# Optimization experiments

Hardware: AMD Instinct MI355X
Metric: run time of the kernel (lower is better)

Reference implementation:

```python
import jax, jax.numpy as jnp
import numpy as np
from jax import lax

C = 320
GN_GROUPS = 32
EPS = 1e-5


def setup_inputs() -> dict:
    key = jax.random.key(0)
    ks = jax.random.split(key, 5)
    x = jax.random.normal(ks[0], (16, C, 96, 96), dtype=jnp.float32)
    # depthwise 3x3 kernel [C,1,3,3] (OIHW with feature_group_count=C)
    dw_w = jax.random.normal(ks[1], (C, 1, 3, 3), dtype=jnp.float32) * 0.1
    dw_b = jax.random.normal(ks[2], (C,), dtype=jnp.float32) * 0.01
    gn_w = jnp.ones((C,), dtype=jnp.float32)
    gn_b = jnp.zeros((C,), dtype=jnp.float32)
    proj_w = jax.random.normal(ks[3], (C,), dtype=jnp.float32) * 0.001
    proj_b = jnp.full((1,), -4.0, dtype=jnp.float32)
    return {"x": x, "dw_w": dw_w, "dw_b": dw_b, "gn_w": gn_w,
            "gn_b": gn_b, "proj_w": proj_w, "proj_b": proj_b}


def _group_norm(h, gamma, beta):
    # h: [B,C,H,W]; GN over (C//G, H, W) within each of G groups; biased var (torch)
    B, Cc, H, W = h.shape
    hg = h.reshape(B, GN_GROUPS, Cc // GN_GROUPS, H, W)
    mean = jnp.mean(hg, axis=(2, 3, 4), keepdims=True)
    var = jnp.mean(jnp.square(hg - mean), axis=(2, 3, 4), keepdims=True)
    hn = ((hg - mean) * lax.rsqrt(var + EPS)).reshape(B, Cc, H, W)
    return hn * gamma[None, :, None, None] + beta[None, :, None, None]


def reference(x, dw_w, dw_b, gn_w, gn_b, proj_w, proj_b):
    # depthwise 3x3 conv, padding=1
    h = lax.conv_general_dilated(
        x, dw_w, window_strides=(1, 1), padding=((1, 1), (1, 1)),
        dimension_numbers=("NCHW", "OIHW", "NCHW"), feature_group_count=C)
    h = h + dw_b[None, :, None, None]
    h = _group_norm(h, gn_w, gn_b)
    # 1x1 conv C -> 1 == per-pixel channel dot product
    g = jnp.einsum("bchw,c->bhw", h, proj_w) + proj_b[0]
    return jax.nn.sigmoid(g)[:, None, :, :]  # [B,1,H,W]
```

## Files before the change

kernel.cpp:

```cpp
#include <hip/hip_runtime.h>
#include <math.h>

#define HH 96
#define WW 96
#define NPIX (HH*WW)
#define CC 320
#define GG 32
#define CPG 10
#define TPB 512

typedef _Float16 half4v __attribute__((ext_vector_type(4)));

__global__ __launch_bounds__(TPB, 4)
void k_main(const float* __restrict__ x, const float* __restrict__ dw_w,
            const float* __restrict__ dw_b, const float* __restrict__ gn_w,
            const float* __restrict__ proj_w,
            _Float16* __restrict__ P, float* __restrict__ partials) {
  const int gr = blockIdx.x & 31;
  const int b  = blockIdx.x >> 5;

  __shared__ float wsm[CPG * 9], ssm[CPG], bsm[CPG];
  const int tid = threadIdx.x;
  if (tid < CPG * 9) wsm[tid] = dw_w[gr * CPG * 9 + tid];
  if (tid < CPG) {
    int c = gr * CPG + tid;
    ssm[tid] = proj_w[c] * gn_w[c];
    bsm[tid] = dw_b[c];
  }
  __syncthreads();

  const int lane = tid & 63;
  const int xcl  = tid & 31;
  const int r    = tid >> 5;
  const bool active = xcl < 24;
  const float mact  = active ? 1.f : 0.f;
  const int xc = min(xcl, 23);
  const float mlft = (xcl > 0)  ? 1.f : 0.f;
  const float mrgt = (xcl < 23) ? 1.f : 0.f;
  const int lm1 = (xcl >= 1) ? lane - 1 : lane;
  const int lp1 = (xcl < 31) ? lane + 1 : lane;

  const float mtop = (r > 0)  ? 1.f : 0.f;
  const float mbot = (r < 15) ? 1.f : 0.f;

  int offs[8];
  #pragma unroll
  for (int k = 0; k < 8; ++k) {
    int yy = min(max(6 * r - 1 + k, 0), HH - 1);
    offs[k] = yy * WW + xc * 4;
  }
  const float* xg = x + ((size_t)(b * CC + gr * CPG)) * NPIX;

  float p[24];
  #pragma unroll
  for (int i = 0; i < 24; ++i) p[i] = 0.f;
  float s1 = 0.f, s2 = 0.f;

  #pragma unroll 1
  for (int ch = 0; ch < CPG; ++ch) {
    const float* img = xg + ch * NPIX;

    float4 R[8];
    #pragma unroll
    for (int k = 0; k < 8; ++k) R[k] = *(const float4*)(img + offs[k]);
    R[0].x *= mtop; R[0].y *= mtop; R[0].z *= mtop; R[0].w *= mtop;
    R[7].x *= mbot; R[7].y *= mbot; R[7].z *= mbot; R[7].w *= mbot;

    float L[8], T[8];
    #pragma unroll
    for (int k = 0; k < 8; ++k) {
      L[k] = __shfl(R[k].w, lm1) * mlft;
      T[k] = __shfl(R[k].x, lp1) * mrgt;
    }

    const float* wp = &wsm[ch * 9];
    const float w0 = wp[0], w1 = wp[1], w2 = wp[2];
    const float w3 = wp[3], w4 = wp[4], w5 = wp[5];
    const float w6 = wp[6], w7 = wp[7], w8 = wp[8];
    const float sc = ssm[ch], bias = bsm[ch];

    #pragma unroll
    for (int j = 0; j < 6; ++j) {
      const float4 A = R[j], B = R[j + 1], C = R[j + 2];
      const float la = L[j], lb = L[j + 1], lc = L[j + 2];
      const float ta = T[j], tb = T[j + 1], tc = T[j + 2];

      float u0 = w0*la  + w1*A.x + w2*A.y + w3*lb  + w4*B.x + w5*B.y + w6*lc  + w7*C.x + w8*C.y;
      float u1 = w0*A.x + w1*A.y + w2*A.z + w3*B.x + w4*B.y + w5*B.z + w6*C.x + w7*C.y + w8*C.z;
      float u2 = w0*A.y + w1*A.z + w2*A.w + w3*B.y + w4*B.z + w5*B.w + w6*C.y + w7*C.z + w8*C.w;
      float u3 = w0*A.z + w1*A.w + w2*ta  + w3*B.z + w4*B.w + w5*tb  + w6*C.z + w7*C.w + w8*tc;

      p[j*4+0] = fmaf(sc, u0, p[j*4+0]);
      p[j*4+1] = fmaf(sc, u1, p[j*4+1]);
      p[j*4+2] = fmaf(sc, u2, p[j*4+2]);
      p[j*4+3] = fmaf(sc, u3, p[j*4+3]);

      float h0 = u0 + bias, h1 = u1 + bias, h2 = u2 + bias, h3 = u3 + bias;
      s1 += mact * ((h0 + h1) + (h2 + h3));
      s2 += mact * (fmaf(h0, h0, h1 * h1) + fmaf(h2, h2, h3 * h3));
    }
  }

  if (active) {
    _Float16* Pp = P + ((size_t)(b * GG + gr)) * NPIX;
    #pragma unroll
    for (int j = 0; j < 6; ++j) {
      half4v h;
      h.x = (_Float16)p[j*4+0]; h.y = (_Float16)p[j*4+1];
      h.z = (_Float16)p[j*4+2]; h.w = (_Float16)p[j*4+3];
      *(half4v*)&Pp[(size_t)(6 * r + j) * WW + xcl * 4] = h;
    }
  }

  #pragma unroll
  for (int off = 32; off; off >>= 1) {
    s1 += __shfl_down(s1, off);
    s2 += __shfl_down(s2, off);
  }
  __shared__ float r1[8], r2[8];
  if ((tid & 63) == 0) { r1[tid >> 6] = s1; r2[tid >> 6] = s2; }
  __syncthreads();
  if (tid == 0) {
    float a = 0.f, q = 0.f;
    #pragma unroll
    for (int i = 0; i < 8; ++i) { a += r1[i]; q += r2[i]; }
    partials[blockIdx.x * 2]     = a;
    partials[blockIdx.x * 2 + 1] = q;
  }
}

__global__ __launch_bounds__(128)
void k_out(const _Float16* __restrict__ P, const float* __restrict__ partials,
           const float* __restrict__ dw_b, const float* __restrict__ gn_w,
           const float* __restrict__ gn_b, const float* __restrict__ proj_w,
           const float* __restrict__ proj_b, float* __restrict__ out) {
  const int b   = blockIdx.x / 18;
  const int blk = blockIdx.x % 18;
  __shared__ float rs[GG];
  __shared__ float Ds;

  if (threadIdx.x < GG) {
    const int gr = threadIdx.x;
    float s1 = partials[(b * GG + gr) * 2];
    float s2 = partials[(b * GG + gr) * 2 + 1];
    const float invN = 1.f / (float)(CPG * NPIX);
    float mean = s1 * invN;
    float var  = s2 * invN - mean * mean;
    float rinv = rsqrtf(var + 1e-5f);
    rs[gr] = rinv;
    float K = 0.f, E = 0.f;
    #pragma unroll
    for (int i = 0; i < CPG; ++i) {
      int c = gr * CPG + i;
      float pg = proj_w[c] * gn_w[c];
      K = fmaf(pg, dw_b[c] - mean, K);
      E = fmaf(proj_w[c], gn_b[c], E);
    }
    float contrib = fmaf(rinv, K, E);
    #pragma unroll
    for (int m = 16; m; m >>= 1) contrib += __shfl_xor(contrib, m, 32);
    if (gr == 0) Ds = contrib + proj_b[0];
  }
  __syncthreads();

  const int p = (blk * 128 + threadIdx.x) * 4;
  const _Float16* Pb = P + (size_t)b * GG * NPIX + p;
  float g0 = 0.f, g1 = 0.f, g2 = 0.f, g3 = 0.f;
  #pragma unroll
  for (int gr = 0; gr < GG; ++gr) {
    half4v v = *(const half4v*)(Pb + (size_t)gr * NPIX);
    float rr = rs[gr];
    g0 = fmaf(rr, (float)v.x, g0);
    g1 = fmaf(rr, (float)v.y, g1);
    g2 = fmaf(rr, (float)v.z, g2);
    g3 = fmaf(rr, (float)v.w, g3);
  }
  const float d = Ds;
  float4 o;
  o.x = 1.f / (1.f + expf(-(g0 + d)));
  o.y = 1.f / (1.f + expf(-(g1 + d)));
  o.z = 1.f / (1.f + expf(-(g2 + d)));
  o.w = 1.f / (1.f + expf(-(g3 + d)));
  *(float4*)&out[(size_t)b * NPIX + p] = o;
}

extern "C" void kernel_launch(void* const* d_in, const int* in_sizes, int n_in,
                              void* d_out, int out_size, void* d_ws, size_t ws_size,
                              hipStream_t stream) {
  const float* x      = (const float*)d_in[0];
  const float* dw_w   = (const float*)d_in[1];
  const float* dw_b   = (const float*)d_in[2];
  const float* gn_w   = (const float*)d_in[3];
  const float* gn_b   = (const float*)d_in[4];
  const float* proj_w = (const float*)d_in[5];
  const float* proj_b = (const float*)d_in[6];
  float* out = (float*)d_out;

  const size_t P_BYTES = (size_t)16 * GG * NPIX * 2;
  _Float16* P     = (_Float16*)d_ws;
  float* partials = (float*)((char*)d_ws + P_BYTES);

  hipLaunchKernelGGL(k_main, dim3(16 * GG), dim3(TPB), 0, stream,
                     x, dw_w, dw_b, gn_w, proj_w, P, partials);
  hipLaunchKernelGGL(k_out, dim3(16 * 18), dim3(128), 0, stream,
                     P, partials, dw_b, gn_w, gn_b, proj_w, proj_b, out);
}
```

Measured before the change: 52.21 us.

## Fuse main and output kernels with a global atomic grid barrier

Merges the two kernels into one and separates the stages with a device-wide atomic counter barrier, which a memset resets before each launch. After the barrier every block computes the group-norm scale factors for its batch and writes 288 output pixels. This removes the second launch and its tail gap. It depends on all 512 blocks being co-resident to avoid deadlock, and the output phase now reads fp16 values as scalars instead of half4 vectors.

After: 146.6 us. 181% more time.

```diff
diff --git a/kernel.cpp b/kernel.cpp
--- a/kernel.cpp
+++ b/kernel.cpp
@@ -8,18 +8,25 @@
 #define GG 32
 #define CPG 10
 #define TPB 512
+#define NBLK (16*GG)
 
 typedef _Float16 half4v __attribute__((ext_vector_type(4)));
 
 __global__ __launch_bounds__(TPB, 4)
-void k_main(const float* __restrict__ x, const float* __restrict__ dw_w,
-            const float* __restrict__ dw_b, const float* __restrict__ gn_w,
-            const float* __restrict__ proj_w,
-            _Float16* __restrict__ P, float* __restrict__ partials) {
+void k_fused(const float* __restrict__ x, const float* __restrict__ dw_w,
+             const float* __restrict__ dw_b, const float* __restrict__ gn_w,
+             const float* __restrict__ gn_b, const float* __restrict__ proj_w,
+             const float* __restrict__ proj_b,
+             _Float16* __restrict__ P, float* __restrict__ partials,
+             unsigned int* __restrict__ bar, float* __restrict__ out) {
   const int gr = blockIdx.x & 31;
   const int b  = blockIdx.x >> 5;
 
   __shared__ float wsm[CPG * 9], ssm[CPG], bsm[CPG];
+  __shared__ float r1[8], r2[8];
+  __shared__ float rs[GG];
+  __shared__ float Ds;
+
   const int tid = threadIdx.x;
   if (tid < CPG * 9) wsm[tid] = dw_w[gr * CPG * 9 + tid];
   if (tid < CPG) {
@@ -39,7 +46,6 @@
   const float mrgt = (xcl < 23) ? 1.f : 0.f;
   const int lm1 = (xcl >= 1) ? lane - 1 : lane;
   const int lp1 = (xcl < 31) ? lane + 1 : lane;
-
   const float mtop = (r > 0)  ? 1.f : 0.f;
   const float mbot = (r < 15) ? 1.f : 0.f;
 
@@ -59,7 +65,6 @@
   #pragma unroll 1
   for (int ch = 0; ch < CPG; ++ch) {
     const float* img = xg + ch * NPIX;
-
     float4 R[8];
     #pragma unroll
     for (int k = 0; k < 8; ++k) R[k] = *(const float4*)(img + offs[k]);
@@ -117,7 +122,6 @@
     s1 += __shfl_down(s1, off);
     s2 += __shfl_down(s2, off);
   }
-  __shared__ float r1[8], r2[8];
   if ((tid & 63) == 0) { r1[tid >> 6] = s1; r2[tid >> 6] = s2; }
   __syncthreads();
   if (tid == 0) {
@@ -127,31 +131,31 @@
     partials[blockIdx.x * 2]     = a;
     partials[blockIdx.x * 2 + 1] = q;
   }
-}
-
-__global__ __launch_bounds__(128)
-void k_out(const _Float16* __restrict__ P, const float* __restrict__ partials,
-           const float* __restrict__ dw_b, const float* __restrict__ gn_w,
-           const float* __restrict__ gn_b, const float* __restrict__ proj_w,
-           const float* __restrict__ proj_b, float* __restrict__ out) {
-  const int b   = blockIdx.x / 18;
-  const int blk = blockIdx.x % 18;
-  __shared__ float rs[GG];
-  __shared__ float Ds;
-
-  if (threadIdx.x < GG) {
-    const int gr = threadIdx.x;
-    float s1 = partials[(b * GG + gr) * 2];
-    float s2 = partials[(b * GG + gr) * 2 + 1];
+
+  __syncthreads();
+  if (tid == 0) {
+    __threadfence();
+    __hip_atomic_fetch_add(bar, 1u, __ATOMIC_RELEASE, __HIP_MEMORY_SCOPE_AGENT);
+    while (__hip_atomic_load(bar, __ATOMIC_ACQUIRE, __HIP_MEMORY_SCOPE_AGENT)
+           < (unsigned)NBLK) {
+      __builtin_amdgcn_s_sleep(2);
+    }
+  }
+  __syncthreads();
+
+  if (tid < GG) {
+    const int g2 = tid;
+    float t1 = partials[(b * GG + g2) * 2];
+    float t2 = partials[(b * GG + g2) * 2 + 1];
     const float invN = 1.f / (float)(CPG * NPIX);
-    float mean = s1 * invN;
-    float var  = s2 * invN - mean * mean;
+    float mean = t1 * invN;
+    float var  = t2 * invN - mean * mean;
     float rinv = rsqrtf(var + 1e-5f);
-    rs[gr] = rinv;
+    rs[g2] = rinv;
     float K = 0.f, E = 0.f;
     #pragma unroll
     for (int i = 0; i < CPG; ++i) {
-      int c = gr * CPG + i;
+      int c = g2 * CPG + i;
       float pg = proj_w[c] * gn_w[c];
       K = fmaf(pg, dw_b[c] - mean, K);
       E = fmaf(proj_w[c], gn_b[c], E);
@@ -159,29 +163,20 @@
     float contrib = fmaf(rinv, K, E);
     #pragma unroll
     for (int m = 16; m; m >>= 1) contrib += __shfl_xor(contrib, m, 32);
-    if (gr == 0) Ds = contrib + proj_b[0];
-  }
-  __syncthreads();
-
-  const int p = (blk * 128 + threadIdx.x) * 4;
-  const _Float16* Pb = P + (size_t)b * GG * NPIX + p;
-  float g0 = 0.f, g1 = 0.f, g2 = 0.f, g3 = 0.f;
-  #pragma unroll
-  for (int gr = 0; gr < GG; ++gr) {
-    half4v v = *(const half4v*)(Pb + (size_t)gr * NPIX);
-    float rr = rs[gr];
-    g0 = fmaf(rr, (float)v.x, g0);
-    g1 = fmaf(rr, (float)v.y, g1);
-    g2 = fmaf(rr, (float)v.z, g2);
-    g3 = fmaf(rr, (float)v.w, g3);
-  }
-  const float d = Ds;
-  float4 o;
-  o.x = 1.f / (1.f + expf(-(g0 + d)));
-  o.y = 1.f / (1.f + expf(-(g1 + d)));
-  o.z = 1.f / (1.f + expf(-(g2 + d)));
-  o.w = 1.f / (1.f + expf(-(g3 + d)));
-  *(float4*)&out[(size_t)b * NPIX + p] = o;
+    if (g2 == 0) Ds = contrib + proj_b[0];
+  }
+  __syncthreads();
+
+  if (tid < 288) {
+    const int px = gr * 288 + tid;
+    const _Float16* Pb = P + (size_t)b * GG * NPIX + px;
+    float g = 0.f;
+    #pragma unroll
+    for (int g2 = 0; g2 < GG; ++g2)
+      g = fmaf(rs[g2], (float)Pb[(size_t)g2 * NPIX], g);
+    g += Ds;
+    out[(size_t)b * NPIX + px] = 1.f / (1.f + expf(-g));
+  }
 }
 
 extern "C" void kernel_launch(void* const* d_in, const int* in_sizes, int n_in,
@@ -197,11 +192,13 @@
   float* out = (float*)d_out;
 
   const size_t P_BYTES = (size_t)16 * GG * NPIX * 2;
-  _Float16* P     = (_Float16*)d_ws;
-  float* partials = (float*)((char*)d_ws + P_BYTES);
-
-  hipLaunchKernelGGL(k_main, dim3(16 * GG), dim3(TPB), 0, stream,
-                     x, dw_w, dw_b, gn_w, proj_w, P, partials);
-  hipLaunchKernelGGL(k_out, dim3(16 * 18), dim3(128), 0, stream,
-                     P, partials, dw_b, gn_w, gn_b, proj_w, proj_b, out);
+  _Float16* P         = (_Float16*)d_ws;
+  float* partials     = (float*)((char*)d_ws + P_BYTES);
+  unsigned int* bar   = (unsigned int*)((char*)d_ws + P_BYTES + 8192);
+
+  hipMemsetAsync((void*)bar, 0, 64, stream);
+
+  hipLaunchKernelGGL(k_fused, dim3(NBLK), dim3(TPB), 0, stream,
+                     x, dw_w, dw_b, gn_w, gn_b, proj_w, proj_b,
+                     P, partials, bar, out);
 }
```
